# Kernel optimization log

Measured on AMD Instinct MI355X. Metric: run time of the kernel, lower is better.

The kernel has to match this reference:

```python
import jax, jax.numpy as jnp
import numpy as np
import math

D_MODEL = 1024
NUM_HEADS = 16
D_K = D_MODEL // NUM_HEADS
MAX_LEN = 512
B, S = 16, 512


def setup_inputs() -> dict:
    key = jax.random.key(0)
    ks = jax.random.split(key, 12)
    init = lambda k, shape, s=0.02: jax.random.normal(k, shape, dtype=jnp.float32) * s
    return {
        "query": jax.random.normal(ks[0], (B, S, D_MODEL), dtype=jnp.float32),
        "key": jax.random.normal(ks[1], (B, S, D_MODEL), dtype=jnp.float32),
        "value": jax.random.normal(ks[2], (B, S, D_MODEL), dtype=jnp.float32),
        "wq_w": init(ks[3], (D_MODEL, D_MODEL)),
        "wq_b": jnp.zeros((D_MODEL,), jnp.float32),
        "wk_w": init(ks[4], (D_MODEL, D_MODEL)),
        "wk_b": jnp.zeros((D_MODEL,), jnp.float32),
        "wv_w": init(ks[5], (D_MODEL, D_MODEL)),
        "wv_b": jnp.zeros((D_MODEL,), jnp.float32),
        "wo_w": init(ks[6], (D_MODEL, D_MODEL)),
        "wo_b": jnp.zeros((D_MODEL,), jnp.float32),
        "rel_bias": init(ks[7], (NUM_HEADS, MAX_LEN, MAX_LEN)),
    }


def reference(query, key, value, wq_w, wq_b, wk_w, wk_b, wv_w, wv_b, wo_w, wo_b, rel_bias):
    b, s, _ = query.shape
    scale = math.sqrt(D_K)
    # torch Linear: x @ W.T + b ; split heads -> [b, s, H, dk]
    Q = (query @ wq_w.T + wq_b).reshape(b, s, NUM_HEADS, D_K)
    K = (key @ wk_w.T + wk_b).reshape(b, s, NUM_HEADS, D_K)
    V = (value @ wv_w.T + wv_b).reshape(b, s, NUM_HEADS, D_K)
    # scores [b, H, s, t]
    scores = jnp.einsum("bshd,bthd->bhst", Q, K) / scale
    scores = scores + rel_bias[None, :, :s, :s]
    causal = jnp.triu(jnp.ones((s, s), dtype=bool), k=1)  # True above diagonal
    scores = jnp.where(causal[None, None, :, :], -jnp.inf, scores)
    attn = jax.nn.softmax(scores, axis=-1)  # dropout p=0 (eval)
    ctx = jnp.einsum("bhst,bthd->bshd", attn, V).reshape(b, s, D_MODEL)
    out = ctx @ wo_w.T + wo_b
    return out, attn.mean(axis=1)
```

## Files before the change

### kernel.cpp

```cpp
#include <hip/hip_runtime.h>
#include <hip/hip_bf16.h>
#include <math.h>

#define D_MODEL 1024
#define NUM_HEADS 16
#define D_K 64
#define BATCH 16
#define SEQ 512

typedef __attribute__((ext_vector_type(8))) short short8;
typedef __attribute__((ext_vector_type(4))) float floatx4;

__device__ inline unsigned short f2bf(float f) {
  __hip_bfloat16 h = __float2bfloat16(f);
  return *reinterpret_cast<unsigned short*>(&h);
}
__device__ inline float bf2f(unsigned short us) {
  unsigned u = ((unsigned)us) << 16;
  return __uint_as_float(u);
}

typedef const __attribute__((address_space(1))) unsigned int glb_u32;
typedef __attribute__((address_space(3))) unsigned int lds_u32;

__device__ inline void load16_to_lds(const void* g, void* l) {
  __builtin_amdgcn_global_load_lds((glb_u32*)(uintptr_t)g,
                                   (lds_u32*)(unsigned int)(uintptr_t)l, 16, 0,
                                   0);
}

__global__ __launch_bounds__(256) void conv_all(
    const float* __restrict__ q, const float* __restrict__ k,
    const float* __restrict__ v, const float* __restrict__ w0,
    const float* __restrict__ w1, const float* __restrict__ w2,
    const float* __restrict__ w3, unsigned short* __restrict__ xq,
    unsigned short* __restrict__ xk, unsigned short* __restrict__ xv,
    unsigned short* __restrict__ d0, unsigned short* __restrict__ d1,
    unsigned short* __restrict__ d2, unsigned short* __restrict__ d3) {
  const size_t MG = 1048576, WG = 131072;
  const size_t g = (size_t)blockIdx.x * 256 + threadIdx.x;
  const float* src;
  unsigned short* dst;
  size_t idx;
  if (g < 3 * MG) {
    const int r = (int)(g >> 20);
    idx = g & (MG - 1);
    src = (r == 0) ? q : (r == 1) ? k : v;
    dst = (r == 0) ? xq : (r == 1) ? xk : xv;
  } else {
    const size_t gw = g - 3 * MG;
    const int r = (int)(gw >> 17);
    idx = gw & (WG - 1);
    src = (r == 0) ? w0 : (r == 1) ? w1 : (r == 2) ? w2 : w3;
    dst = (r == 0) ? d0 : (r == 1) ? d1 : (r == 2) ? d2 : d3;
  }
  const float4 a = ((const float4*)src)[2 * idx];
  const float4 b = ((const float4*)src)[2 * idx + 1];
  short8 o;
  o[0] = f2bf(a.x); o[1] = f2bf(a.y); o[2] = f2bf(a.z); o[3] = f2bf(a.w);
  o[4] = f2bf(b.x); o[5] = f2bf(b.y); o[6] = f2bf(b.z); o[7] = f2bf(b.w);
  ((short8*)dst)[idx] = o;
}

__global__ __launch_bounds__(256) void qkv_gemm(
    const unsigned short* __restrict__ Xall,
    const unsigned short* __restrict__ Wall,
    const float* __restrict__ bq, const float* __restrict__ bk,
    const float* __restrict__ bv,
    unsigned short* __restrict__ QKout,
    unsigned short* __restrict__ Vt) {
  constexpr int K = 1024;
  const size_t ME = (size_t)BATCH * SEQ * D_MODEL;
  const size_t WE = (size_t)D_MODEL * D_MODEL;

  const int f = blockIdx.x + (blockIdx.y << 3) + (blockIdx.z << 9);
  const int virt = ((f & 7) * 192) + (f >> 3);
  const int xi = virt & 7;
  const int rest = virt >> 3;
  const int yi = rest & 63;
  const int z = rest >> 6;

  const unsigned short* A = Xall + (size_t)z * ME;
  const unsigned short* Bw = Wall + (size_t)z * WE;
  const float* bias = (z == 0) ? bq : (z == 1) ? bk : bv;

  __shared__ __align__(16) unsigned short sA[128 * 64];
  __shared__ __align__(16) unsigned short sB[128 * 64];
  const int tid = threadIdx.x;
  const int w = tid >> 6, lane = tid & 63;
  const int quad = lane >> 4, lq = lane & 15;
  const int wm = w >> 1, wn = w & 1;
  const int m0 = yi << 7, n0 = xi << 7;

  const int lrow8 = lane >> 3;
  const int sg = lane & 7;

  floatx4 acc[4][4];
#pragma unroll
  for (int i = 0; i < 4; ++i)
#pragma unroll
    for (int j = 0; j < 4; ++j) acc[i][j] = {0.f, 0.f, 0.f, 0.f};

  for (int kt = 0; kt < K; kt += 64) {
    __syncthreads();
#pragma unroll
    for (int i = 0; i < 4; ++i) {
      const int row = (i << 5) + (w << 3) + lrow8;
      const int g = sg ^ (row & 7);
      const unsigned short* gA = A + (size_t)(m0 + row) * K + kt + (g << 3);
      const unsigned short* gB = Bw + (size_t)(n0 + row) * K + kt + (g << 3);
      unsigned short* lA = &sA[(((i << 5) + (w << 3))) * 64];
      unsigned short* lB = &sB[(((i << 5) + (w << 3))) * 64];
      load16_to_lds(gA, lA);
      load16_to_lds(gB, lB);
    }
    __syncthreads();
#pragma unroll
    for (int s = 0; s < 2; ++s) {
      short8 aF[4], bF[4];
#pragma unroll
      for (int mi = 0; mi < 4; ++mi) {
        const int row = (wm << 6) + (mi << 4) + lq;
        const int g = ((s << 2) + quad) ^ (row & 7);
        aF[mi] = *(const short8*)&sA[row * 64 + (g << 3)];
      }
#pragma unroll
      for (int ni = 0; ni < 4; ++ni) {
        const int row = (wn << 6) + (ni << 4) + lq;
        const int g = ((s << 2) + quad) ^ (row & 7);
        bF[ni] = *(const short8*)&sB[row * 64 + (g << 3)];
      }
#pragma unroll
      for (int mi = 0; mi < 4; ++mi)
#pragma unroll
        for (int ni = 0; ni < 4; ++ni)
          acc[mi][ni] = __builtin_amdgcn_mfma_f32_16x16x32_bf16(
              aF[mi], bF[ni], acc[mi][ni], 0, 0, 0);
    }
  }

#pragma unroll
  for (int ni = 0; ni < 4; ++ni) {
    const int n = n0 + (wn << 6) + (ni << 4) + lq;
    const float bn = bias[n];
    const int hh = n >> 6, dk = n & 63;
#pragma unroll
    for (int mi = 0; mi < 4; ++mi) {
      const int mb = m0 + (wm << 6) + (mi << 4) + (quad << 2);
      const int bb = mb >> 9, ss = mb & 511;
      if (z == 2) {
        ushort4 pk;
        pk.x = f2bf(acc[mi][ni][0] + bn);
        pk.y = f2bf(acc[mi][ni][1] + bn);
        pk.z = f2bf(acc[mi][ni][2] + bn);
        pk.w = f2bf(acc[mi][ni][3] + bn);
        *(ushort4*)&Vt[((size_t)(bb * NUM_HEADS + hh) * D_K + dk) * SEQ + ss] =
            pk;
      } else {
        unsigned short* dst = QKout + (size_t)z * ME;
#pragma unroll
        for (int r = 0; r < 4; ++r)
          dst[((size_t)(bb * NUM_HEADS + hh) * SEQ + ss + r) * D_K + dk] =
              f2bf(acc[mi][ni][r] + bn);
      }
    }
  }
}

__global__ __launch_bounds__(256) void out_gemm(
    const unsigned short* __restrict__ A, const unsigned short* __restrict__ Bw,
    const float* __restrict__ bias, float* __restrict__ Cout) {
  constexpr int K = 1024;
  __shared__ __align__(16) unsigned short sA[128 * 64];
  __shared__ __align__(16) unsigned short sB[128 * 64];
  const int tid = threadIdx.x;
  const int w = tid >> 6, lane = tid & 63;
  const int quad = lane >> 4, lq = lane & 15;
  const int wm = w >> 1, wn = w & 1;

  const int f = blockIdx.x + (blockIdx.y << 3);
  const int virt = ((f & 7) << 6) + (f >> 3);
  const int m0 = (virt >> 3) << 7, n0 = (virt & 7) << 7;

  const int lrow8 = lane >> 3;
  const int sg = lane & 7;

  floatx4 acc[4][4];
#pragma unroll
  for (int i = 0; i < 4; ++i)
#pragma unroll
    for (int j = 0; j < 4; ++j) acc[i][j] = {0.f, 0.f, 0.f, 0.f};

  for (int kt = 0; kt < K; kt += 64) {
    __syncthreads();
#pragma unroll
    for (int i = 0; i < 4; ++i) {
      const int row = (i << 5) + (w << 3) + lrow8;
      const int g = sg ^ (row & 7);
      const unsigned short* gA = A + (size_t)(m0 + row) * K + kt + (g << 3);
      const unsigned short* gB = Bw + (size_t)(n0 + row) * K + kt + (g << 3);
      unsigned short* lA = &sA[(((i << 5) + (w << 3))) * 64];
      unsigned short* lB = &sB[(((i << 5) + (w << 3))) * 64];
      load16_to_lds(gA, lA);
      load16_to_lds(gB, lB);
    }
    __syncthreads();
#pragma unroll
    for (int s = 0; s < 2; ++s) {
      short8 aF[4], bF[4];
#pragma unroll
      for (int mi = 0; mi < 4; ++mi) {
        const int row = (wm << 6) + (mi << 4) + lq;
        const int g = ((s << 2) + quad) ^ (row & 7);
        aF[mi] = *(const short8*)&sA[row * 64 + (g << 3)];
      }
#pragma unroll
      for (int ni = 0; ni < 4; ++ni) {
        const int row = (wn << 6) + (ni << 4) + lq;
        const int g = ((s << 2) + quad) ^ (row & 7);
        bF[ni] = *(const short8*)&sB[row * 64 + (g << 3)];
      }
#pragma unroll
      for (int mi = 0; mi < 4; ++mi)
#pragma unroll
        for (int ni = 0; ni < 4; ++ni)
          acc[mi][ni] = __builtin_amdgcn_mfma_f32_16x16x32_bf16(
              aF[mi], bF[ni], acc[mi][ni], 0, 0, 0);
    }
  }

#pragma unroll
  for (int ni = 0; ni < 4; ++ni) {
    const int n = n0 + (wn << 6) + (ni << 4) + lq;
    const float bn = bias[n];
#pragma unroll
    for (int mi = 0; mi < 4; ++mi) {
      const int mb = m0 + (wm << 6) + (mi << 4) + (quad << 2);
#pragma unroll
      for (int r = 0; r < 4; ++r)
        Cout[(size_t)(mb + r) * 1024 + n] = acc[mi][ni][r] + bn;
    }
  }
}

__global__ __launch_bounds__(512) void attn_mfma(
    const unsigned short* __restrict__ Qb,
    const unsigned short* __restrict__ Kb,
    const unsigned short* __restrict__ Vt,
    const float* __restrict__ rb,
    unsigned short* __restrict__ ctxb,
    unsigned short* __restrict__ Pg,
    float* __restrict__ flWS) {
  const int b = blockIdx.x;
  const int h = blockIdx.y;
  const int tid = threadIdx.x;
  const int w = tid >> 6, lane = tid & 63;
  const int quad = lane >> 4, lq = lane & 15;

  __shared__ __align__(16) unsigned short sK[512 * 64];
  __shared__ __align__(16) unsigned short sV[64 * 512];
  __shared__ __align__(16) unsigned short sPt[8][16][72];

  const size_t bh = (size_t)b * NUM_HEADS + h;
  const unsigned short* Qh = Qb + bh * SEQ * D_K;
  const unsigned short* Kh = Kb + bh * SEQ * D_K;
  const unsigned short* Vh = Vt + bh * D_K * SEQ;
  const float* rbh = rb + (size_t)h * SEQ * SEQ;

#pragma unroll
  for (int it = 0; it < 8; ++it) {
    const int L = (it << 13) + (tid << 4);
    {
      const int rk = L >> 7, ck = (L >> 4) & 7;
      load16_to_lds(
          (const unsigned char*)Kh + (L & ~127) + ((ck ^ (rk & 7)) << 4),
          (unsigned char*)sK + L);
    }
    {
      const int rv = L >> 10, cv = (L >> 4) & 63;
      load16_to_lds(
          (const unsigned char*)Vh + (L & ~1023) + ((cv ^ (rv & 7)) << 4),
          (unsigned char*)sV + L);
    }
  }
  __syncthreads();

#pragma unroll 1
  for (int si = 0; si < 4; ++si) {
    const int st = (si == 0) ? w : (si == 1) ? (15 - w)
                 : (si == 2) ? (16 + w) : (31 - w);
    const int qs = st << 4;
    const int nc = (st >> 2) + 1;

    short8 aQ0, aQ1;
    {
      const unsigned short* qrow = Qh + (size_t)(qs + lq) * D_K + (quad << 3);
      aQ0 = *(const short8*)(qrow);
      aQ1 = *(const short8*)(qrow + 32);
    }

    float lsum[4] = {0.f, 0.f, 0.f, 0.f};
    floatx4 O[4] = {{0.f, 0.f, 0.f, 0.f},
                    {0.f, 0.f, 0.f, 0.f},
                    {0.f, 0.f, 0.f, 0.f},
                    {0.f, 0.f, 0.f, 0.f}};

    const float* rbbase = rbh + (size_t)(qs + (quad << 2)) * SEQ + lq;
    float rbv[16];
#pragma unroll
    for (int nt = 0; nt < 4; ++nt)
#pragma unroll
      for (int r = 0; r < 4; ++r)
        rbv[nt * 4 + r] = rbbase[(size_t)r * SEQ + (nt << 4)];

    for (int c = 0; c < nc; ++c) {
      const int t0 = c << 6;
      float rbn[16];
      if (c + 1 < nc) {
        const float* rn = rbbase + t0 + 64;
#pragma unroll
        for (int nt = 0; nt < 4; ++nt)
#pragma unroll
          for (int r = 0; r < 4; ++r)
            rbn[nt * 4 + r] = rn[(size_t)r * SEQ + (nt << 4)];
      }

#pragma unroll
      for (int nt = 0; nt < 4; ++nt) {
        const int kr = t0 + (nt << 4) + lq;
        const unsigned char* kbase = (const unsigned char*)sK + (kr << 7);
        short8 bK0 = *(const short8*)(kbase + ((quad ^ (kr & 7)) << 4));
        short8 bK1 = *(const short8*)(kbase + (((quad + 4) ^ (kr & 7)) << 4));
        floatx4 s = {0.f, 0.f, 0.f, 0.f};
        s = __builtin_amdgcn_mfma_f32_16x16x32_bf16(aQ0, bK0, s, 0, 0, 0);
        s = __builtin_amdgcn_mfma_f32_16x16x32_bf16(aQ1, bK1, s, 0, 0, 0);
        const int col = t0 + (nt << 4) + lq;
#pragma unroll
        for (int r = 0; r < 4; ++r) {
          const int row = qs + (quad << 2) + r;
          float p = 0.f;
          if (col <= row) p = __expf(s[r] * 0.125f + rbv[nt * 4 + r]);
          lsum[r] += p;
          sPt[w][(quad << 2) + r][(nt << 4) + lq] = f2bf(p);
        }
      }

      short8 bV0[4], bV1[4];
#pragma unroll
      for (int nt = 0; nt < 4; ++nt) {
        const int vr = (nt << 4) + lq;
        const unsigned char* vbase = (const unsigned char*)sV + (vr << 10);
        const int cc = (t0 >> 3) + quad;
        bV0[nt] = *(const short8*)(vbase + ((cc ^ (vr & 7)) << 4));
        bV1[nt] = *(const short8*)(vbase + (((cc + 4) ^ (vr & 7)) << 4));
      }

      short8 aP0 = *(const short8*)&sPt[w][lq][quad << 3];
      short8 aP1 = *(const short8*)&sPt[w][lq][32 + (quad << 3)];

      {
        unsigned short* pgrow =
            Pg + (bh * SEQ + (qs + lq)) * SEQ + t0 + (quad << 3);
        *(short8*)pgrow = aP0;
        *(short8*)(pgrow + 32) = aP1;
      }

#pragma unroll
      for (int nt = 0; nt < 4; ++nt) {
        O[nt] = __builtin_amdgcn_mfma_f32_16x16x32_bf16(aP0, bV0[nt], O[nt], 0,
                                                        0, 0);
        O[nt] = __builtin_amdgcn_mfma_f32_16x16x32_bf16(aP1, bV1[nt], O[nt], 0,
                                                        0, 0);
      }

      if (c + 1 < nc) {
#pragma unroll
        for (int i = 0; i < 16; ++i) rbv[i] = rbn[i];
      }
    }

#pragma unroll
    for (int off = 1; off < 16; off <<= 1)
#pragma unroll
      for (int r = 0; r < 4; ++r) lsum[r] += __shfl_xor(lsum[r], off);
    float invl[4];
#pragma unroll
    for (int r = 0; r < 4; ++r) invl[r] = 1.f / lsum[r];
    if (lq == 0) {
#pragma unroll
      for (int r = 0; r < 4; ++r)
        flWS[bh * SEQ + qs + (quad << 2) + r] = invl[r] * 0.0625f;
    }
#pragma unroll
    for (int nt = 0; nt < 4; ++nt)
#pragma unroll
      for (int r = 0; r < 4; ++r) {
        const int row = qs + (quad << 2) + r;
        ctxb[((size_t)b * SEQ + row) * D_MODEL + h * D_K + (nt << 4) + lq] =
            f2bf(O[nt][r] * invl[r]);
      }
  }
}

__global__ __launch_bounds__(256) void attn_reduce(
    const unsigned short* __restrict__ Pg, const float* __restrict__ flWS,
    float* __restrict__ attn_mean) {
  const int b = blockIdx.x, rt = blockIdx.y, cs = blockIdx.z;
#pragma unroll
  for (int k = 0; k < 4; ++k) {
    const int slot = threadIdx.x + (k << 8);
    const int row = (rt << 6) + (slot >> 4);
    const int col0 = (cs << 7) + ((slot & 15) << 3);
    float acc[8] = {0.f, 0.f, 0.f, 0.f, 0.f, 0.f, 0.f, 0.f};
    if (col0 <= row) {
      for (int h = 0; h < NUM_HEADS; ++h) {
        const size_t base = (((size_t)b * NUM_HEADS + h) << 9) + row;
        const float f = flWS[base];
        const uint4 pk = *(const uint4*)&Pg[(base << 9) + col0];
        acc[0] += bf2f((unsigned short)(pk.x & 0xffff)) * f;
        acc[1] += bf2f((unsigned short)(pk.x >> 16)) * f;
        acc[2] += bf2f((unsigned short)(pk.y & 0xffff)) * f;
        acc[3] += bf2f((unsigned short)(pk.y >> 16)) * f;
        acc[4] += bf2f((unsigned short)(pk.z & 0xffff)) * f;
        acc[5] += bf2f((unsigned short)(pk.z >> 16)) * f;
        acc[6] += bf2f((unsigned short)(pk.w & 0xffff)) * f;
        acc[7] += bf2f((unsigned short)(pk.w >> 16)) * f;
      }
    }
    float4 o0, o1;
    o0.x = (col0 + 0 <= row) ? acc[0] : 0.f;
    o0.y = (col0 + 1 <= row) ? acc[1] : 0.f;
    o0.z = (col0 + 2 <= row) ? acc[2] : 0.f;
    o0.w = (col0 + 3 <= row) ? acc[3] : 0.f;
    o1.x = (col0 + 4 <= row) ? acc[4] : 0.f;
    o1.y = (col0 + 5 <= row) ? acc[5] : 0.f;
    o1.z = (col0 + 6 <= row) ? acc[6] : 0.f;
    o1.w = (col0 + 7 <= row) ? acc[7] : 0.f;
    float* dst = attn_mean + (((size_t)b << 9) + row) * SEQ + col0;
    *(float4*)dst = o0;
    *(float4*)(dst + 4) = o1;
  }
}

extern "C" void kernel_launch(void* const* d_in, const int* in_sizes, int n_in,
                              void* d_out, int out_size, void* d_ws,
                              size_t ws_size, hipStream_t stream) {
  const float* query = (const float*)d_in[0];
  const float* key_ = (const float*)d_in[1];
  const float* value = (const float*)d_in[2];
  const float* wq_w = (const float*)d_in[3];
  const float* wq_b = (const float*)d_in[4];
  const float* wk_w = (const float*)d_in[5];
  const float* wk_b = (const float*)d_in[6];
  const float* wv_w = (const float*)d_in[7];
  const float* wv_b = (const float*)d_in[8];
  const float* wo_w = (const float*)d_in[9];
  const float* wo_b = (const float*)d_in[10];
  const float* rel_bias = (const float*)d_in[11];

  float* out = (float*)d_out;
  float* attn_mean = out + (size_t)BATCH * SEQ * D_MODEL;

  const size_t ME = (size_t)BATCH * SEQ * D_MODEL;
  const size_t WE = (size_t)D_MODEL * D_MODEL;
  const size_t RE = (size_t)BATCH * NUM_HEADS * SEQ;

  unsigned short* Qb = (unsigned short*)d_ws;
  unsigned short* Kb = Qb + ME;
  unsigned short* Vt = Kb + ME;
  unsigned short* ctxb = Vt + ME;
  unsigned short* wob = ctxb + ME;
  float* flWS = (float*)(wob + WE);
  unsigned short* Pg = (unsigned short*)(flWS + RE);
  unsigned short* xq = Pg;
  unsigned short* xk = xq + ME;
  unsigned short* xv = xk + ME;
  unsigned short* wqb = xv + ME;
  unsigned short* wkb = wqb + WE;
  unsigned short* wvb = wkb + WE;

  conv_all<<<14336, 256, 0, stream>>>(query, key_, value, wq_w, wk_w, wv_w,
                                      wo_w, xq, xk, xv, wqb, wkb, wvb, wob);

  dim3 qkvg(8, 64, 3);
  qkv_gemm<<<qkvg, 256, 0, stream>>>(xq, wqb, wq_b, wk_b, wv_b, Qb, Vt);

  dim3 agrid(BATCH, NUM_HEADS);
  attn_mfma<<<agrid, 512, 0, stream>>>(Qb, Kb, Vt, rel_bias, ctxb, Pg, flWS);

  dim3 rgrid(BATCH, 8, 4);
  attn_reduce<<<rgrid, 256, 0, stream>>>(Pg, flWS, attn_mean);

  dim3 gblk(8, 64);
  out_gemm<<<gblk, 256, 0, stream>>>(ctxb, wob, wo_b, out);
}
```

Before: 327.5 us.

## Double-buffer LDS tiles in QKV and output projection GEMMs

Both projection GEMM kernels now keep two LDS buffers per operand. The next K-tile is issued into the alternate buffer before the MFMA work on the current one, and each iteration ends with a single barrier. This aims to overlap global-to-LDS loads with matrix math and halve the barriers per iteration. In exchange the kernels use twice the shared memory, which may reduce occupancy. Correctness depends on the async LDS loads being complete by the trailing barrier.

After: 316.6 us. 3.3% less time.

```diff
diff --git a/kernel.cpp b/kernel.cpp
--- a/kernel.cpp
+++ b/kernel.cpp
@@ -84,8 +84,8 @@
   const unsigned short* Bw = Wall + (size_t)z * WE;
   const float* bias = (z == 0) ? bq : (z == 1) ? bk : bv;
 
-  __shared__ __align__(16) unsigned short sA[128 * 64];
-  __shared__ __align__(16) unsigned short sB[128 * 64];
+  __shared__ __align__(16) unsigned short sA[2][128 * 64];
+  __shared__ __align__(16) unsigned short sB[2][128 * 64];
   const int tid = threadIdx.x;
   const int w = tid >> 6, lane = tid & 63;
   const int quad = lane >> 4, lq = lane & 15;
@@ -101,20 +101,23 @@
 #pragma unroll
     for (int j = 0; j < 4; ++j) acc[i][j] = {0.f, 0.f, 0.f, 0.f};
 
-  for (int kt = 0; kt < K; kt += 64) {
-    __syncthreads();
+  auto stage = [&](int buf, int kt) {
 #pragma unroll
     for (int i = 0; i < 4; ++i) {
       const int row = (i << 5) + (w << 3) + lrow8;
       const int g = sg ^ (row & 7);
       const unsigned short* gA = A + (size_t)(m0 + row) * K + kt + (g << 3);
       const unsigned short* gB = Bw + (size_t)(n0 + row) * K + kt + (g << 3);
-      unsigned short* lA = &sA[(((i << 5) + (w << 3))) * 64];
-      unsigned short* lB = &sB[(((i << 5) + (w << 3))) * 64];
-      load16_to_lds(gA, lA);
-      load16_to_lds(gB, lB);
-    }
-    __syncthreads();
+      load16_to_lds(gA, &sA[buf][((i << 5) + (w << 3)) * 64]);
+      load16_to_lds(gB, &sB[buf][((i << 5) + (w << 3)) * 64]);
+    }
+  };
+
+  stage(0, 0);
+  __syncthreads();
+  int cur = 0;
+  for (int kt = 0; kt < K; kt += 64) {
+    if (kt + 64 < K) stage(cur ^ 1, kt + 64);
 #pragma unroll
     for (int s = 0; s < 2; ++s) {
       short8 aF[4], bF[4];
@@ -122,13 +125,13 @@
       for (int mi = 0; mi < 4; ++mi) {
         const int row = (wm << 6) + (mi << 4) + lq;
         const int g = ((s << 2) + quad) ^ (row & 7);
-        aF[mi] = *(const short8*)&sA[row * 64 + (g << 3)];
+        aF[mi] = *(const short8*)&sA[cur][row * 64 + (g << 3)];
       }
 #pragma unroll
       for (int ni = 0; ni < 4; ++ni) {
         const int row = (wn << 6) + (ni << 4) + lq;
         const int g = ((s << 2) + quad) ^ (row & 7);
-        bF[ni] = *(const short8*)&sB[row * 64 + (g << 3)];
+        bF[ni] = *(const short8*)&sB[cur][row * 64 + (g << 3)];
       }
 #pragma unroll
       for (int mi = 0; mi < 4; ++mi)
@@ -137,6 +140,8 @@
           acc[mi][ni] = __builtin_amdgcn_mfma_f32_16x16x32_bf16(
               aF[mi], bF[ni], acc[mi][ni], 0, 0, 0);
     }
+    __syncthreads();
+    cur ^= 1;
   }
 
 #pragma unroll
@@ -171,8 +176,8 @@
     const unsigned short* __restrict__ A, const unsigned short* __restrict__ Bw,
     const float* __restrict__ bias, float* __restrict__ Cout) {
   constexpr int K = 1024;
-  __shared__ __align__(16) unsigned short sA[128 * 64];
-  __shared__ __align__(16) unsigned short sB[128 * 64];
+  __shared__ __align__(16) unsigned short sA[2][128 * 64];
+  __shared__ __align__(16) unsigned short sB[2][128 * 64];
   const int tid = threadIdx.x;
   const int w = tid >> 6, lane = tid & 63;
   const int quad = lane >> 4, lq = lane & 15;
@@ -191,20 +196,23 @@
 #pragma unroll
     for (int j = 0; j < 4; ++j) acc[i][j] = {0.f, 0.f, 0.f, 0.f};
 
-  for (int kt = 0; kt < K; kt += 64) {
-    __syncthreads();
+  auto stage = [&](int buf, int kt) {
 #pragma unroll
     for (int i = 0; i < 4; ++i) {
       const int row = (i << 5) + (w << 3) + lrow8;
       const int g = sg ^ (row & 7);
       const unsigned short* gA = A + (size_t)(m0 + row) * K + kt + (g << 3);
       const unsigned short* gB = Bw + (size_t)(n0 + row) * K + kt + (g << 3);
-      unsigned short* lA = &sA[(((i << 5) + (w << 3))) * 64];
-      unsigned short* lB = &sB[(((i << 5) + (w << 3))) * 64];
-      load16_to_lds(gA, lA);
-      load16_to_lds(gB, lB);
-    }
-    __syncthreads();
+      load16_to_lds(gA, &sA[buf][((i << 5) + (w << 3)) * 64]);
+      load16_to_lds(gB, &sB[buf][((i << 5) + (w << 3)) * 64]);
+    }
+  };
+
+  stage(0, 0);
+  __syncthreads();
+  int cur = 0;
+  for (int kt = 0; kt < K; kt += 64) {
+    if (kt + 64 < K) stage(cur ^ 1, kt + 64);
 #pragma unroll
     for (int s = 0; s < 2; ++s) {
       short8 aF[4], bF[4];
@@ -212,13 +220,13 @@
       for (int mi = 0; mi < 4; ++mi) {
         const int row = (wm << 6) + (mi << 4) + lq;
         const int g = ((s << 2) + quad) ^ (row & 7);
-        aF[mi] = *(const short8*)&sA[row * 64 + (g << 3)];
+        aF[mi] = *(const short8*)&sA[cur][row * 64 + (g << 3)];
       }
 #pragma unroll
       for (int ni = 0; ni < 4; ++ni) {
         const int row = (wn << 6) + (ni << 4) + lq;
         const int g = ((s << 2) + quad) ^ (row & 7);
-        bF[ni] = *(const short8*)&sB[row * 64 + (g << 3)];
+        bF[ni] = *(const short8*)&sB[cur][row * 64 + (g << 3)];
       }
 #pragma unroll
       for (int mi = 0; mi < 4; ++mi)
@@ -227,6 +235,8 @@
           acc[mi][ni] = __builtin_amdgcn_mfma_f32_16x16x32_bf16(
               aF[mi], bF[ni], acc[mi][ni], 0, 0, 0);
     }
+    __syncthreads();
+    cur ^= 1;
   }
 
 #pragma unroll
```
